# Performance work log

Hardware: AMD Instinct MI355X
Metric: run time of the kernel (lower is better)

Reference implementation:

```python
import jax, jax.numpy as jnp
import numpy as np

TEMP = 0.1        # ds_temperature
THRESHOLD = 0.2
MARGIN = 2        # margin_remove


def setup_inputs() -> dict:
    key = jax.random.key(0)
    k0, k1 = jax.random.split(key)
    N, C = 2, 256
    h0, w0, h1, w1 = 60, 80, 60, 80
    feature0 = jax.random.normal(k0, (N, h0 * w0, C), dtype=jnp.float32)
    feature1 = jax.random.normal(k1, (N, h1 * w1, C), dtype=jnp.float32)
    return {"feature0": feature0, "feature1": feature1,
            "h0": h0, "w0": w0, "h1": h1, "w1": w1}


def _interior(n: int, b: int) -> jnp.ndarray:
    # True on [b, n-b), mirroring mask[:, :b]=False and mask[:, -b:]=False
    a = jnp.arange(n)
    return (a >= b) & (a < n - b)


def reference(feature0, feature1, h0, w0, h1, w1):
    N, L, C = feature0.shape
    S = feature1.shape[1]
    # similarities: (f0/sqrt(C)) . (f1/sqrt(C)) / temp == f0.f1 / (C*temp)
    sim = jnp.einsum('nlc,nsc->nls', feature0, feature1) / (C * TEMP)
    # dual softmax confidences
    conf = jax.nn.softmax(sim, axis=2) * jax.nn.softmax(sim, axis=1)
    # threshold mask with spatial margin removal (mask0 is None branch)
    mask = conf > THRESHOLD                      # [N, L, S]
    m5 = mask.reshape(N, h0, w0, h1, w1)
    valid = (_interior(h0, MARGIN)[:, None, None, None]
             & _interior(w0, MARGIN)[None, :, None, None]
             & _interior(h1, MARGIN)[None, None, :, None]
             & _interior(w1, MARGIN)[None, None, None, :])
    m5 = m5 & valid[None]
    mask = m5.reshape(N, L, S)
    # mutual nearest neighbor constraint
    mutual = ((conf == conf.max(axis=2, keepdims=True))
              & (conf == conf.max(axis=1, keepdims=True)))
    mask = mask & mutual
    # dense (jit-safe) encoding of the matches: confidences zeroed off-match.
    matched_conf = jnp.where(mask, conf, 0.0)
    return conf, mask, matched_conf
```

## Files before the change

### kernel.cpp

```cpp
#include <hip/hip_runtime.h>

#define NB 2
#define LD 4800
#define SD 4800
#define CD 256
#define H0 60
#define W0 80
#define H1 60
#define W1 80
#define MG 2
#define THRESH 0.2f
#define SIM_SCALE (1.0f / (256.0f * 0.1f))

typedef float f32x4 __attribute__((ext_vector_type(4)));
typedef __bf16 bf16x8 __attribute__((ext_vector_type(8)));
typedef unsigned short u16x8 __attribute__((ext_vector_type(8)));

__device__ __forceinline__ unsigned short f2bf(float f) {
    unsigned int u = __float_as_uint(f);
    u = u + 0x7FFFu + ((u >> 16) & 1u);
    return (unsigned short)(u >> 16);
}

__device__ __forceinline__ bool interior0(int idx) {
    int i = idx / W0, j = idx % W0;
    return (i >= MG) & (i < H0 - MG) & (j >= MG) & (j < W0 - MG);
}
__device__ __forceinline__ bool interior1(int idx) {
    int i = idx / W1, j = idx % W1;
    return (i >= MG) & (i < H1 - MG) & (j >= MG) & (j < W1 - MG);
}

__global__ __launch_bounds__(256) void k_zero(float* __restrict__ p, int n) {
    int i = blockIdx.x * 256 + threadIdx.x;
    if (i < n) p[i] = 0.f;
}

__global__ __launch_bounds__(256) void k_gemm(const float* __restrict__ f0,
                                              const float* __restrict__ f1,
                                              float* __restrict__ sim,
                                              float* __restrict__ rowsum,
                                              float* __restrict__ colsum) {
    __shared__ __align__(16) unsigned short As[128][40];
    __shared__ __align__(16) unsigned short Bs[128][40];

    const int n  = blockIdx.z;
    const int s0 = blockIdx.x * 128;
    const int l0 = blockIdx.y * 128;
    const int tid  = threadIdx.x;
    const int lane = tid & 63;
    const int wave = tid >> 6;
    const int wm = (wave >> 1) * 64;
    const int wn = (wave & 1) * 64;
    const int quad = lane >> 4;
    const int lr   = lane & 15;

    f32x4 acc[4][4];
#pragma unroll
    for (int i = 0; i < 4; ++i)
#pragma unroll
        for (int j = 0; j < 4; ++j) acc[i][j] = (f32x4){0.f, 0.f, 0.f, 0.f};

    const int r  = tid >> 1;
    const int c0 = (tid & 1) * 16;
    const bool a_ok = (l0 + r) < LD;
    const bool b_ok = (s0 + r) < SD;
    const float* aptr = f0 + ((size_t)n * LD + (a_ok ? (l0 + r) : 0)) * CD + c0;
    const float* bptr = f1 + ((size_t)n * SD + (b_ok ? (s0 + r) : 0)) * CD + c0;

    for (int k0 = 0; k0 < CD; k0 += 32) {
        __syncthreads();
        float4 da[4], db[4];
#pragma unroll
        for (int v = 0; v < 4; ++v) {
            da[v] = a_ok ? *(const float4*)(aptr + k0 + 4 * v) : make_float4(0, 0, 0, 0);
            db[v] = b_ok ? *(const float4*)(bptr + k0 + 4 * v) : make_float4(0, 0, 0, 0);
        }
        u16x8 va0 = {f2bf(da[0].x), f2bf(da[0].y), f2bf(da[0].z), f2bf(da[0].w),
                     f2bf(da[1].x), f2bf(da[1].y), f2bf(da[1].z), f2bf(da[1].w)};
        u16x8 va1 = {f2bf(da[2].x), f2bf(da[2].y), f2bf(da[2].z), f2bf(da[2].w),
                     f2bf(da[3].x), f2bf(da[3].y), f2bf(da[3].z), f2bf(da[3].w)};
        u16x8 vb0 = {f2bf(db[0].x), f2bf(db[0].y), f2bf(db[0].z), f2bf(db[0].w),
                     f2bf(db[1].x), f2bf(db[1].y), f2bf(db[1].z), f2bf(db[1].w)};
        u16x8 vb1 = {f2bf(db[2].x), f2bf(db[2].y), f2bf(db[2].z), f2bf(db[2].w),
                     f2bf(db[3].x), f2bf(db[3].y), f2bf(db[3].z), f2bf(db[3].w)};
        *(u16x8*)&As[r][c0]     = va0;
        *(u16x8*)&As[r][c0 + 8] = va1;
        *(u16x8*)&Bs[r][c0]     = vb0;
        *(u16x8*)&Bs[r][c0 + 8] = vb1;
        __syncthreads();

        bf16x8 af[4], bfr[4];
#pragma unroll
        for (int i = 0; i < 4; ++i) {
            af[i]  = __builtin_bit_cast(bf16x8, *(const u16x8*)&As[wm + i * 16 + lr][quad * 8]);
            bfr[i] = __builtin_bit_cast(bf16x8, *(const u16x8*)&Bs[wn + i * 16 + lr][quad * 8]);
        }
#pragma unroll
        for (int i = 0; i < 4; ++i)
#pragma unroll
            for (int j = 0; j < 4; ++j)
                acc[i][j] = __builtin_amdgcn_mfma_f32_16x16x32_bf16(af[i], bfr[j], acc[i][j], 0, 0, 0);
    }

    const int rb = l0 + wm;
    const int cb = s0 + wn;
    float rpart[4][4];
    float cpart[4];
#pragma unroll
    for (int i = 0; i < 4; ++i) {
        cpart[i] = 0.f;
#pragma unroll
        for (int g = 0; g < 4; ++g) rpart[i][g] = 0.f;
    }
#pragma unroll
    for (int mi = 0; mi < 4; ++mi)
#pragma unroll
        for (int ni = 0; ni < 4; ++ni)
#pragma unroll
            for (int g = 0; g < 4; ++g) {
                int row = rb + mi * 16 + quad * 4 + g;
                int col = cb + ni * 16 + lr;
                float sv = acc[mi][ni][g] * SIM_SCALE;
                bool ok = (row < LD) & (col < SD);
                float ev = ok ? __expf(sv) : 0.f;
                rpart[mi][g] += ev;
                cpart[ni] += ev;
                if (ok) sim[((size_t)n * LD + row) * SD + col] = sv;
            }
#pragma unroll
    for (int mi = 0; mi < 4; ++mi)
#pragma unroll
        for (int g = 0; g < 4; ++g) {
            float v = rpart[mi][g];
            v += __shfl_xor(v, 1);
            v += __shfl_xor(v, 2);
            v += __shfl_xor(v, 4);
            v += __shfl_xor(v, 8);
            int row = rb + mi * 16 + quad * 4 + g;
            if (lr == 0 && row < LD) atomicAdd(&rowsum[n * LD + row], v);
        }
#pragma unroll
    for (int ni = 0; ni < 4; ++ni) {
        float v = cpart[ni];
        v += __shfl_xor(v, 16);
        v += __shfl_xor(v, 32);
        int col = cb + ni * 16 + lr;
        if (quad == 0 && col < SD) atomicAdd(&colsum[n * SD + col], v);
    }
}

__global__ __launch_bounds__(256) void k_conf(float* __restrict__ conf,
                                              const float* __restrict__ rowsum,
                                              const float* __restrict__ colsum,
                                              float* __restrict__ rowmax) {
    const int l = blockIdx.x, n = blockIdx.y;
    const size_t base = ((size_t)n * LD + l) * SD;
    const float rinv = 1.0f / rowsum[n * LD + l];
    const float* cs = colsum + (size_t)n * SD;
    float m = 0.f;
    for (int s = threadIdx.x * 4; s < SD; s += 1024) {
        float4 sv = *(const float4*)(conf + base + s);
        float4 c4 = *(const float4*)(cs + s);
        float4 o;
        o.x = __expf(2.f * sv.x) * rinv / c4.x;
        o.y = __expf(2.f * sv.y) * rinv / c4.y;
        o.z = __expf(2.f * sv.z) * rinv / c4.z;
        o.w = __expf(2.f * sv.w) * rinv / c4.w;
        *(float4*)(conf + base + s) = o;
        m = fmaxf(m, fmaxf(fmaxf(o.x, o.y), fmaxf(o.z, o.w)));
    }
#pragma unroll
    for (int off = 32; off; off >>= 1) m = fmaxf(m, __shfl_xor(m, off));
    __shared__ float red[4];
    if ((threadIdx.x & 63) == 0) red[threadIdx.x >> 6] = m;
    __syncthreads();
    if (threadIdx.x == 0)
        rowmax[n * LD + l] = fmaxf(fmaxf(red[0], red[1]), fmaxf(red[2], red[3]));
}

__global__ __launch_bounds__(256) void k_colmax(const float* __restrict__ conf,
                                                unsigned int* __restrict__ colmax) {
    const int n = blockIdx.z;
    const int s = (blockIdx.x * 256 + threadIdx.x) * 4;
    if (s >= SD) return;
    const int l0 = blockIdx.y * 75;
    const float* p = conf + ((size_t)n * LD + l0) * SD + s;
    float4 m = {0.f, 0.f, 0.f, 0.f};
    for (int i = 0; i < 75; ++i) {
        float4 v = *(const float4*)(p + (size_t)i * SD);
        m.x = fmaxf(m.x, v.x);
        m.y = fmaxf(m.y, v.y);
        m.z = fmaxf(m.z, v.z);
        m.w = fmaxf(m.w, v.w);
    }
    unsigned int* c = colmax + (size_t)n * SD + s;
    atomicMax(c + 0, __float_as_uint(m.x));
    atomicMax(c + 1, __float_as_uint(m.y));
    atomicMax(c + 2, __float_as_uint(m.z));
    atomicMax(c + 3, __float_as_uint(m.w));
}

__global__ __launch_bounds__(256) void k_final(const float* __restrict__ conf,
                                               const float* __restrict__ rowmax,
                                               const float* __restrict__ colmax,
                                               float* __restrict__ mask,
                                               float* __restrict__ matched) {
    const int l = blockIdx.x, n = blockIdx.y;
    const size_t base = ((size_t)n * LD + l) * SD;
    const bool v0 = interior0(l);
    const float rm = rowmax[n * LD + l];
    const float* cm = colmax + (size_t)n * SD;
    for (int s = threadIdx.x * 4; s < SD; s += 1024) {
        float4 c = *(const float4*)(conf + base + s);
        float4 x = *(const float4*)(cm + s);
        float4 mk, mt;
        {
            bool b = v0 & (c.x > THRESH) & interior1(s + 0) & (c.x == rm) & (c.x == x.x);
            mk.x = b ? 1.f : 0.f; mt.x = b ? c.x : 0.f;
        }
        {
            bool b = v0 & (c.y > THRESH) & interior1(s + 1) & (c.y == rm) & (c.y == x.y);
            mk.y = b ? 1.f : 0.f; mt.y = b ? c.y : 0.f;
        }
        {
            bool b = v0 & (c.z > THRESH) & interior1(s + 2) & (c.z == rm) & (c.z == x.z);
            mk.z = b ? 1.f : 0.f; mt.z = b ? c.z : 0.f;
        }
        {
            bool b = v0 & (c.w > THRESH) & interior1(s + 3) & (c.w == rm) & (c.w == x.w);
            mk.w = b ? 1.f : 0.f; mt.w = b ? c.w : 0.f;
        }
        *(float4*)(mask + base + s) = mk;
        *(float4*)(matched + base + s) = mt;
    }
}

extern "C" void kernel_launch(void* const* d_in, const int* in_sizes, int n_in,
                              void* d_out, int out_size, void* d_ws, size_t ws_size,
                              hipStream_t stream) {
    const float* f0 = (const float*)d_in[0];
    const float* f1 = (const float*)d_in[1];
    const size_t plane = (size_t)NB * LD * SD;
    float* conf = (float*)d_out;
    float* mask = conf + plane;
    float* matched = mask + plane;

    float* rowsum = (float*)d_ws;
    float* colsum = rowsum + NB * LD;
    unsigned int* colmax = (unsigned int*)(colsum + NB * SD);
    float* rowmax = (float*)(colmax + NB * SD);

    k_zero<<<dim3((NB * (LD + SD + SD) + 255) / 256), 256, 0, stream>>>(rowsum,
                                                                        NB * (LD + SD + SD));
    k_gemm<<<dim3((SD + 127) / 128, (LD + 127) / 128, NB), 256, 0, stream>>>(
        f0, f1, conf, rowsum, colsum);
    k_conf<<<dim3(LD, NB), 256, 0, stream>>>(conf, rowsum, colsum, rowmax);
    k_colmax<<<dim3(5, 64, NB), 256, 0, stream>>>(conf, colmax);
    k_final<<<dim3(LD, NB), 256, 0, stream>>>(conf, rowmax, (const float*)colmax, mask, matched);
}
```

Before: 763.5 us.

## Recompute GEMM in two passes to fuse softmax conf and row/col max

Features are pre-converted to bf16 once, with the output mask buffer reused as scratch, and the GEMM tiles are loaded straight into LDS via global_load_lds. The GEMM now runs twice. The first pass only accumulates exp row and column sums. The second pass recomputes the similarities, writes conf directly, and atomically reduces row and column maxima. This removes the full sim-matrix write, the separate conf read-modify-write kernel and the colmax read pass over the 184MB plane, at the cost of doubling the GEMM compute and adding conversion kernels.

```diff
diff --git a/kernel.cpp b/kernel.cpp
--- a/kernel.cpp
+++ b/kernel.cpp
@@ -11,10 +11,19 @@
 #define MG 2
 #define THRESH 0.2f
 #define SIM_SCALE (1.0f / (256.0f * 0.1f))
+#define GT 38
 
 typedef float f32x4 __attribute__((ext_vector_type(4)));
 typedef __bf16 bf16x8 __attribute__((ext_vector_type(8)));
 typedef unsigned short u16x8 __attribute__((ext_vector_type(8)));
+
+#define GLOBAL_AS __attribute__((address_space(1)))
+#define LDS_AS __attribute__((address_space(3)))
+
+__device__ __forceinline__ void gl_lds16(const unsigned short* g, unsigned short* l) {
+    __builtin_amdgcn_global_load_lds((const GLOBAL_AS unsigned int*)g,
+                                     (LDS_AS unsigned int*)l, 16, 0, 0);
+}
 
 __device__ __forceinline__ unsigned short f2bf(float f) {
     unsigned int u = __float_as_uint(f);
@@ -36,13 +45,27 @@
     if (i < n) p[i] = 0.f;
 }
 
-__global__ __launch_bounds__(256) void k_gemm(const float* __restrict__ f0,
-                                              const float* __restrict__ f1,
-                                              float* __restrict__ sim,
+__global__ __launch_bounds__(256) void k_cvt(const float* __restrict__ src,
+                                             unsigned short* __restrict__ dst, int n8) {
+    int i = blockIdx.x * 256 + threadIdx.x;
+    if (i >= n8) return;
+    const float4* s = (const float4*)src + (size_t)i * 2;
+    float4 a = s[0], b = s[1];
+    u16x8 o = {f2bf(a.x), f2bf(a.y), f2bf(a.z), f2bf(a.w),
+               f2bf(b.x), f2bf(b.y), f2bf(b.z), f2bf(b.w)};
+    *(u16x8*)(dst + (size_t)i * 8) = o;
+}
+
+template <int PASS>
+__global__ __launch_bounds__(256) void k_gemm(const unsigned short* __restrict__ bA,
+                                              const unsigned short* __restrict__ bB,
                                               float* __restrict__ rowsum,
-                                              float* __restrict__ colsum) {
-    __shared__ __align__(16) unsigned short As[128][40];
-    __shared__ __align__(16) unsigned short Bs[128][40];
+                                              float* __restrict__ colsum,
+                                              float* __restrict__ conf,
+                                              unsigned int* __restrict__ rowmax,
+                                              unsigned int* __restrict__ colmax) {
+    __shared__ __align__(16) unsigned short As[128][32];
+    __shared__ __align__(16) unsigned short Bs[128][32];
 
     const int n  = blockIdx.z;
     const int s0 = blockIdx.x * 128;
@@ -55,39 +78,29 @@
     const int quad = lane >> 4;
     const int lr   = lane & 15;
 
+    const int sr = wave * 32 + (lane >> 2);
+    const int sc = (lane & 3) * 8;
+    const unsigned short* ga0 = bA + ((size_t)n * LD + min(l0 + sr,      LD - 1)) * CD + sc;
+    const unsigned short* ga1 = bA + ((size_t)n * LD + min(l0 + sr + 16, LD - 1)) * CD + sc;
+    const unsigned short* gb0 = bB + ((size_t)n * SD + min(s0 + sr,      SD - 1)) * CD + sc;
+    const unsigned short* gb1 = bB + ((size_t)n * SD + min(s0 + sr + 16, SD - 1)) * CD + sc;
+    unsigned short* la0 = &As[wave * 32][0];
+    unsigned short* la1 = &As[wave * 32 + 16][0];
+    unsigned short* lb0 = &Bs[wave * 32][0];
+    unsigned short* lb1 = &Bs[wave * 32 + 16][0];
+
     f32x4 acc[4][4];
 #pragma unroll
     for (int i = 0; i < 4; ++i)
 #pragma unroll
         for (int j = 0; j < 4; ++j) acc[i][j] = (f32x4){0.f, 0.f, 0.f, 0.f};
-
-    const int r  = tid >> 1;
-    const int c0 = (tid & 1) * 16;
-    const bool a_ok = (l0 + r) < LD;
-    const bool b_ok = (s0 + r) < SD;
-    const float* aptr = f0 + ((size_t)n * LD + (a_ok ? (l0 + r) : 0)) * CD + c0;
-    const float* bptr = f1 + ((size_t)n * SD + (b_ok ? (s0 + r) : 0)) * CD + c0;
 
     for (int k0 = 0; k0 < CD; k0 += 32) {
         __syncthreads();
-        float4 da[4], db[4];
-#pragma unroll
-        for (int v = 0; v < 4; ++v) {
-            da[v] = a_ok ? *(const float4*)(aptr + k0 + 4 * v) : make_float4(0, 0, 0, 0);
-            db[v] = b_ok ? *(const float4*)(bptr + k0 + 4 * v) : make_float4(0, 0, 0, 0);
-        }
-        u16x8 va0 = {f2bf(da[0].x), f2bf(da[0].y), f2bf(da[0].z), f2bf(da[0].w),
-                     f2bf(da[1].x), f2bf(da[1].y), f2bf(da[1].z), f2bf(da[1].w)};
-        u16x8 va1 = {f2bf(da[2].x), f2bf(da[2].y), f2bf(da[2].z), f2bf(da[2].w),
-                     f2bf(da[3].x), f2bf(da[3].y), f2bf(da[3].z), f2bf(da[3].w)};
-        u16x8 vb0 = {f2bf(db[0].x), f2bf(db[0].y), f2bf(db[0].z), f2bf(db[0].w),
-                     f2bf(db[1].x), f2bf(db[1].y), f2bf(db[1].z), f2bf(db[1].w)};
-        u16x8 vb1 = {f2bf(db[2].x), f2bf(db[2].y), f2bf(db[2].z), f2bf(db[2].w),
-                     f2bf(db[3].x), f2bf(db[3].y), f2bf(db[3].z), f2bf(db[3].w)};
-        *(u16x8*)&As[r][c0]     = va0;
-        *(u16x8*)&As[r][c0 + 8] = va1;
-        *(u16x8*)&Bs[r][c0]     = vb0;
-        *(u16x8*)&Bs[r][c0 + 8] = vb1;
+        gl_lds16(ga0 + k0, la0);
+        gl_lds16(ga1 + k0, la1);
+        gl_lds16(gb0 + k0, lb0);
+        gl_lds16(gb1 + k0, lb1);
         __syncthreads();
 
         bf16x8 af[4], bfr[4];
@@ -105,100 +118,112 @@
 
     const int rb = l0 + wm;
     const int cb = s0 + wn;
-    float rpart[4][4];
-    float cpart[4];
-#pragma unroll
-    for (int i = 0; i < 4; ++i) {
-        cpart[i] = 0.f;
-#pragma unroll
-        for (int g = 0; g < 4; ++g) rpart[i][g] = 0.f;
+
+    if (PASS == 0) {
+        float rpart[4][4];
+        float cpart[4];
+#pragma unroll
+        for (int i = 0; i < 4; ++i) {
+            cpart[i] = 0.f;
+#pragma unroll
+            for (int g = 0; g < 4; ++g) rpart[i][g] = 0.f;
+        }
+#pragma unroll
+        for (int mi = 0; mi < 4; ++mi)
+#pragma unroll
+            for (int ni = 0; ni < 4; ++ni)
+#pragma unroll
+                for (int g = 0; g < 4; ++g) {
+                    int row = rb + mi * 16 + quad * 4 + g;
+                    int col = cb + ni * 16 + lr;
+                    float sv = acc[mi][ni][g] * SIM_SCALE;
+                    bool ok = (row < LD) & (col < SD);
+                    float ev = ok ? __expf(sv) : 0.f;
+                    rpart[mi][g] += ev;
+                    cpart[ni] += ev;
+                }
+#pragma unroll
+        for (int mi = 0; mi < 4; ++mi)
+#pragma unroll
+            for (int g = 0; g < 4; ++g) {
+                float v = rpart[mi][g];
+                v += __shfl_xor(v, 1);
+                v += __shfl_xor(v, 2);
+                v += __shfl_xor(v, 4);
+                v += __shfl_xor(v, 8);
+                int row = rb + mi * 16 + quad * 4 + g;
+                if (lr == 0 && row < LD) atomicAdd(&rowsum[n * LD + row], v);
+            }
+#pragma unroll
+        for (int ni = 0; ni < 4; ++ni) {
+            float v = cpart[ni];
+            v += __shfl_xor(v, 16);
+            v += __shfl_xor(v, 32);
+            int col = cb + ni * 16 + lr;
+            if (quad == 0 && col < SD) atomicAdd(&colsum[n * SD + col], v);
+        }
+    } else {
+        float rinv[4][4], cinv[4];
+#pragma unroll
+        for (int mi = 0; mi < 4; ++mi)
+#pragma unroll
+            for (int g = 0; g < 4; ++g) {
+                int row = min(rb + mi * 16 + quad * 4 + g, LD - 1);
+                rinv[mi][g] = 1.0f / rowsum[n * LD + row];
+            }
+#pragma unroll
+        for (int ni = 0; ni < 4; ++ni) {
+            int col = min(cb + ni * 16 + lr, SD - 1);
+            cinv[ni] = 1.0f / colsum[n * SD + col];
+        }
+        float rmx[4][4], cmx[4];
+#pragma unroll
+        for (int i = 0; i < 4; ++i) {
+            cmx[i] = 0.f;
+#pragma unroll
+            for (int g = 0; g < 4; ++g) rmx[i][g] = 0.f;
+        }
+#pragma unroll
+        for (int mi = 0; mi < 4; ++mi)
+#pragma unroll
+            for (int ni = 0; ni < 4; ++ni)
+#pragma unroll
+                for (int g = 0; g < 4; ++g) {
+                    int row = rb + mi * 16 + quad * 4 + g;
+                    int col = cb + ni * 16 + lr;
+                    float sv = acc[mi][ni][g] * SIM_SCALE;
+                    float e = __expf(sv);
+                    float cv = e * e * rinv[mi][g] * cinv[ni];
+                    bool ok = (row < LD) & (col < SD);
+                    if (ok) {
+                        conf[((size_t)n * LD + row) * SD + col] = cv;
+                        rmx[mi][g] = fmaxf(rmx[mi][g], cv);
+                        cmx[ni]    = fmaxf(cmx[ni], cv);
+                    }
+                }
+#pragma unroll
+        for (int mi = 0; mi < 4; ++mi)
+#pragma unroll
+            for (int g = 0; g < 4; ++g) {
+                float v = rmx[mi][g];
+                v = fmaxf(v, __shfl_xor(v, 1));
+                v = fmaxf(v, __shfl_xor(v, 2));
+                v = fmaxf(v, __shfl_xor(v, 4));
+                v = fmaxf(v, __shfl_xor(v, 8));
+                int row = rb + mi * 16 + quad * 4 + g;
+                if (lr == 0 && row < LD)
+                    atomicMax(&rowmax[n * LD + row], __float_as_uint(v));
+            }
+#pragma unroll
+        for (int ni = 0; ni < 4; ++ni) {
+            float v = cmx[ni];
+            v = fmaxf(v, __shfl_xor(v, 16));
+            v = fmaxf(v, __shfl_xor(v, 32));
+            int col = cb + ni * 16 + lr;
+            if (quad == 0 && col < SD)
+                atomicMax(&colmax[n * SD + col], __float_as_uint(v));
+        }
     }
-#pragma unroll
-    for (int mi = 0; mi < 4; ++mi)
-#pragma unroll
-        for (int ni = 0; ni < 4; ++ni)
-#pragma unroll
-            for (int g = 0; g < 4; ++g) {
-                int row = rb + mi * 16 + quad * 4 + g;
-                int col = cb + ni * 16 + lr;
-                float sv = acc[mi][ni][g] * SIM_SCALE;
-                bool ok = (row < LD) & (col < SD);
-                float ev = ok ? __expf(sv) : 0.f;
-                rpart[mi][g] += ev;
-                cpart[ni] += ev;
-                if (ok) sim[((size_t)n * LD + row) * SD + col] = sv;
-            }
-#pragma unroll
-    for (int mi = 0; mi < 4; ++mi)
-#pragma unroll
-        for (int g = 0; g < 4; ++g) {
-            float v = rpart[mi][g];
-            v += __shfl_xor(v, 1);
-            v += __shfl_xor(v, 2);
-            v += __shfl_xor(v, 4);
-            v += __shfl_xor(v, 8);
-            int row = rb + mi * 16 + quad * 4 + g;
-            if (lr == 0 && row < LD) atomicAdd(&rowsum[n * LD + row], v);
-        }
-#pragma unroll
-    for (int ni = 0; ni < 4; ++ni) {
-        float v = cpart[ni];
-        v += __shfl_xor(v, 16);
-        v += __shfl_xor(v, 32);
-        int col = cb + ni * 16 + lr;
-        if (quad == 0 && col < SD) atomicAdd(&colsum[n * SD + col], v);
-    }
-}
-
-__global__ __launch_bounds__(256) void k_conf(float* __restrict__ conf,
-                                              const float* __restrict__ rowsum,
-                                              const float* __restrict__ colsum,
-                                              float* __restrict__ rowmax) {
-    const int l = blockIdx.x, n = blockIdx.y;
-    const size_t base = ((size_t)n * LD + l) * SD;
-    const float rinv = 1.0f / rowsum[n * LD + l];
-    const float* cs = colsum + (size_t)n * SD;
-    float m = 0.f;
-    for (int s = threadIdx.x * 4; s < SD; s += 1024) {
-        float4 sv = *(const float4*)(conf + base + s);
-        float4 c4 = *(const float4*)(cs + s);
-        float4 o;
-        o.x = __expf(2.f * sv.x) * rinv / c4.x;
-        o.y = __expf(2.f * sv.y) * rinv / c4.y;
-        o.z = __expf(2.f * sv.z) * rinv / c4.z;
-        o.w = __expf(2.f * sv.w) * rinv / c4.w;
-        *(float4*)(conf + base + s) = o;
-        m = fmaxf(m, fmaxf(fmaxf(o.x, o.y), fmaxf(o.z, o.w)));
-    }
-#pragma unroll
-    for (int off = 32; off; off >>= 1) m = fmaxf(m, __shfl_xor(m, off));
-    __shared__ float red[4];
-    if ((threadIdx.x & 63) == 0) red[threadIdx.x >> 6] = m;
-    __syncthreads();
-    if (threadIdx.x == 0)
-        rowmax[n * LD + l] = fmaxf(fmaxf(red[0], red[1]), fmaxf(red[2], red[3]));
-}
-
-__global__ __launch_bounds__(256) void k_colmax(const float* __restrict__ conf,
-                                                unsigned int* __restrict__ colmax) {
-    const int n = blockIdx.z;
-    const int s = (blockIdx.x * 256 + threadIdx.x) * 4;
-    if (s >= SD) return;
-    const int l0 = blockIdx.y * 75;
-    const float* p = conf + ((size_t)n * LD + l0) * SD + s;
-    float4 m = {0.f, 0.f, 0.f, 0.f};
-    for (int i = 0; i < 75; ++i) {
-        float4 v = *(const float4*)(p + (size_t)i * SD);
-        m.x = fmaxf(m.x, v.x);
-        m.y = fmaxf(m.y, v.y);
-        m.z = fmaxf(m.z, v.z);
-        m.w = fmaxf(m.w, v.w);
-    }
-    unsigned int* c = colmax + (size_t)n * SD + s;
-    atomicMax(c + 0, __float_as_uint(m.x));
-    atomicMax(c + 1, __float_as_uint(m.y));
-    atomicMax(c + 2, __float_as_uint(m.z));
-    atomicMax(c + 3, __float_as_uint(m.w));
 }
 
 __global__ __launch_bounds__(256) void k_final(const float* __restrict__ conf,
@@ -248,14 +273,21 @@
 
     float* rowsum = (float*)d_ws;
     float* colsum = rowsum + NB * LD;
-    unsigned int* colmax = (unsigned int*)(colsum + NB * SD);
-    float* rowmax = (float*)(colmax + NB * SD);
-
-    k_zero<<<dim3((NB * (LD + SD + SD) + 255) / 256), 256, 0, stream>>>(rowsum,
-                                                                        NB * (LD + SD + SD));
-    k_gemm<<<dim3((SD + 127) / 128, (LD + 127) / 128, NB), 256, 0, stream>>>(
-        f0, f1, conf, rowsum, colsum);
-    k_conf<<<dim3(LD, NB), 256, 0, stream>>>(conf, rowsum, colsum, rowmax);
-    k_colmax<<<dim3(5, 64, NB), 256, 0, stream>>>(conf, colmax);
-    k_final<<<dim3(LD, NB), 256, 0, stream>>>(conf, rowmax, (const float*)colmax, mask, matched);
-}
+    unsigned int* rowmaxu = (unsigned int*)(colsum + NB * SD);
+    unsigned int* colmaxu = rowmaxu + NB * LD;
+
+    unsigned short* bf0 = (unsigned short*)mask;
+    unsigned short* bf1 = bf0 + (size_t)NB * LD * CD;
+
+    const int nstat = NB * (LD + SD + LD + SD);
+    k_zero<<<dim3((nstat + 255) / 256), 256, 0, stream>>>(rowsum, nstat);
+    const int n8 = NB * LD * CD / 8;
+    k_cvt<<<dim3((n8 + 255) / 256), 256, 0, stream>>>(f0, bf0, n8);
+    k_cvt<<<dim3((n8 + 255) / 256), 256, 0, stream>>>(f1, bf1, n8);
+
+    dim3 gg(GT, GT, NB);
+    k_gemm<0><<<gg, 256, 0, stream>>>(bf0, bf1, rowsum, colsum, nullptr, nullptr, nullptr);
+    k_gemm<1><<<gg, 256, 0, stream>>>(bf0, bf1, rowsum, colsum, conf, rowmaxu, colmaxu);
+    k_final<<<dim3(LD, NB), 256, 0, stream>>>(conf, (const float*)rowmaxu,
+                                              (const float*)colmaxu, mask, matched);
+}
```

New measurement: 716.1 us. -6.2%, faster.
